# Kernel optimization log

Measured on AMD Instinct MI355X. Metric: run time of the kernel, lower is better.

## Reference

```python
import jax, jax.numpy as jnp
import numpy as np
from jax import lax

B, T, I, H = 256, 1024, 64, 128  # batch(padded_length), seq_len, input_size, hidden_size


def setup_inputs() -> dict:
    key = jax.random.key(0)
    k0, k1, k2, k3, k4 = jax.random.split(key, 5)
    s = 1.0 / np.sqrt(H)  # pytorch LSTM default init scale
    return {
        "data": jax.random.normal(k0, (B, T, I), dtype=jnp.float32),
        "W_ih": jax.random.uniform(k1, (4 * H, I), dtype=jnp.float32, minval=-s, maxval=s),
        "W_hh": jax.random.uniform(k2, (4 * H, H), dtype=jnp.float32, minval=-s, maxval=s),
        "b_ih": jax.random.uniform(k3, (4 * H,), dtype=jnp.float32, minval=-s, maxval=s),
        "b_hh": jax.random.uniform(k4, (4 * H,), dtype=jnp.float32, minval=-s, maxval=s),
    }


def reference(data, W_ih, W_hh, b_ih, b_hh):
    # data: [B, T, I]. Original permutes to [T, B, I] and runs a per-timestep
    # single-layer LSTM loop with zero initial state, collecting h_t each step.
    b, t, _ = data.shape
    h_dim = W_hh.shape[1]
    # Precompute input projection for all timesteps: [T, B, 4H]
    xs = jnp.einsum('bti,gi->tbg', data, W_ih) + b_ih + b_hh

    def step(carry, x_t):
        h, c = carry
        gates = x_t + h @ W_hh.T  # [B, 4H]
        i, f, g, o = jnp.split(gates, 4, axis=-1)  # pytorch gate order: i,f,g,o
        i = jax.nn.sigmoid(i)
        f = jax.nn.sigmoid(f)
        g = jnp.tanh(g)
        o = jax.nn.sigmoid(o)
        c = f * c + i * g
        h = o * jnp.tanh(c)
        return (h, c), h

    h0 = jnp.zeros((b, h_dim), dtype=data.dtype)
    _, hs = lax.scan(step, (h0, h0), xs)  # hs: [T, B, H]
    return jnp.transpose(hs, (1, 0, 2))  # [B, T, H]
```

## Files before the change

### kernel.cpp

```cpp
#include <hip/hip_runtime.h>


typedef _Float16 half8  __attribute__((ext_vector_type(8)));
typedef _Float16 half2t __attribute__((ext_vector_type(2)));
typedef float  floatx4  __attribute__((ext_vector_type(4)));

constexpr int Tt = 1024;
constexpr int Ii = 64;
constexpr int Hh = 128;
constexpr int CH = 16;
constexpr int NCH = Tt / CH;

__device__ __forceinline__ float fast_rcp(float x) { return __builtin_amdgcn_rcpf(x); }
__device__ __forceinline__ half2t pk16(float a, float b) {
    return __builtin_bit_cast(half2t, __builtin_amdgcn_cvt_pkrtz(a, b));
}
#define MFMA16(A, B, C) __builtin_amdgcn_mfma_f32_16x16x32_f16((A), (B), (C), 0, 0, 0)
union H8U { half8 v; half2t p[4]; };

__global__ __launch_bounds__(512, 2) void lstm_mfma4(
    const float* __restrict__ data,
    const float* __restrict__ W_ih,
    const float* __restrict__ W_hh,
    const float* __restrict__ b_ih,
    const float* __restrict__ b_hh,
    float* __restrict__ out)
{
    const int b   = blockIdx.x;
    const int t   = threadIdx.x;
    const int w   = t >> 6;
    const int l   = t & 63;
    const int col = l & 15;
    const int kg  = l >> 4;

    half8 bfh[4][4];
    half8 bfx[4][2];
    floatx4 bv[4];
#pragma unroll
    for (int g = 0; g < 4; ++g) {
        const int row = 128 * g + 16 * w + col;
        const float bias = b_ih[row] + b_hh[row];
        bv[g][0] = bias; bv[g][1] = bias; bv[g][2] = bias; bv[g][3] = bias;
        const float* wh = W_hh + (size_t)row * Hh;
        const float* wi = W_ih + (size_t)row * Ii;
#pragma unroll
        for (int s = 0; s < 4; ++s) {
            const float* src = wh + 32 * s + 8 * kg;
            const float4 f0 = ((const float4*)src)[0];
            const float4 f1 = ((const float4*)src)[1];
            H8U u;
            u.p[0] = pk16(f0.x, f0.y); u.p[1] = pk16(f0.z, f0.w);
            u.p[2] = pk16(f1.x, f1.y); u.p[3] = pk16(f1.z, f1.w);
            bfh[g][s] = u.v;
        }
#pragma unroll
        for (int s = 0; s < 2; ++s) {
            const float* src = wi + 32 * s + 8 * kg;
            const float4 f0 = ((const float4*)src)[0];
            const float4 f1 = ((const float4*)src)[1];
            H8U u;
            u.p[0] = pk16(f0.x, f0.y); u.p[1] = pk16(f0.z, f0.w);
            u.p[2] = pk16(f1.x, f1.y); u.p[3] = pk16(f1.z, f1.w);
            bfx[g][s] = u.v;
        }
    }

    __shared__ __align__(8) _Float16 hb[2][Hh];

    const float* xp  = data + (size_t)b * Tt * Ii;
    float*       opr = out  + (size_t)b * Tt * Hh + 16 * w + col;

    if (t < Hh) hb[0][t] = (_Float16)0.0f;

    const float* xbase = xp + (size_t)(l & 15) * Ii + 8 * kg;
    float4 xf0 = *(const float4*)(xbase);
    float4 xf1 = *(const float4*)(xbase + 4);
    float4 xf2 = *(const float4*)(xbase + 32);
    float4 xf3 = *(const float4*)(xbase + 36);

    float c = 0.0f;
    __syncthreads();

#pragma unroll 1
    for (int n = 0; n < NCH; ++n) {
        H8U ax0, ax1;
        ax0.p[0] = pk16(xf0.x, xf0.y); ax0.p[1] = pk16(xf0.z, xf0.w);
        ax0.p[2] = pk16(xf1.x, xf1.y); ax0.p[3] = pk16(xf1.z, xf1.w);
        ax1.p[0] = pk16(xf2.x, xf2.y); ax1.p[1] = pk16(xf2.z, xf2.w);
        ax1.p[2] = pk16(xf3.x, xf3.y); ax1.p[3] = pk16(xf3.z, xf3.w);
        floatx4 xw0 = MFMA16(ax0.v, bfx[0][0], bv[0]);
        floatx4 xw1 = MFMA16(ax0.v, bfx[1][0], bv[1]);
        floatx4 xw2 = MFMA16(ax0.v, bfx[2][0], bv[2]);
        floatx4 xw3 = MFMA16(ax0.v, bfx[3][0], bv[3]);
        xw0 = MFMA16(ax1.v, bfx[0][1], xw0);
        xw1 = MFMA16(ax1.v, bfx[1][1], xw1);
        xw2 = MFMA16(ax1.v, bfx[2][1], xw2);
        xw3 = MFMA16(ax1.v, bfx[3][1], xw3);

        {
            const int nn = (n + 1 < NCH) ? (n + 1) : n;
            const float* xb2 = xbase + (size_t)nn * CH * Ii;
            xf0 = *(const float4*)(xb2);
            xf1 = *(const float4*)(xb2 + 4);
            xf2 = *(const float4*)(xb2 + 32);
            xf3 = *(const float4*)(xb2 + 36);
        }

#define STEP(P, R, CUR)                                                       \
        {                                                                     \
            const _Float16* hbase = &hb[CUR][8 * kg];                         \
            const half8 ah0 = *(const half8*)(hbase);                         \
            const half8 ah1 = *(const half8*)(hbase + 32);                    \
            const half8 ah2 = *(const half8*)(hbase + 64);                    \
            const half8 ah3 = *(const half8*)(hbase + 96);                    \
            __builtin_amdgcn_s_setprio(1);                                    \
            floatx4 q0 = MFMA16(ah0, bfh[0][0], xw0);                  \
            floatx4 q2 = MFMA16(ah0, bfh[2][0], xw2);                  \
            q0 = MFMA16(ah1, bfh[0][1], q0);                                  \
            q2 = MFMA16(ah1, bfh[2][1], q2);                                  \
            q0 = MFMA16(ah2, bfh[0][2], q0);                                  \
            q2 = MFMA16(ah2, bfh[2][2], q2);                                  \
            q0 = MFMA16(ah3, bfh[0][3], q0);                                  \
            q2 = MFMA16(ah3, bfh[2][3], q2);                                  \
            floatx4 q1 = MFMA16(ah0, bfh[1][0], xw1);                  \
            floatx4 q3 = MFMA16(ah0, bfh[3][0], xw3);                  \
            const float gi = q0[R], gG = q2[R];                               \
            const float ig = fast_rcp(1.0f + __expf(-gi));                    \
            const float eg = __expf(-2.0f * gG);                              \
            q1 = MFMA16(ah1, bfh[1][1], q1);                                  \
            q3 = MFMA16(ah1, bfh[3][1], q3);                                  \
            const float gv = (1.0f - eg) * fast_rcp(1.0f + eg);               \
            const float igv = ig * gv;                                        \
            q1 = MFMA16(ah2, bfh[1][2], q1);                                  \
            q3 = MFMA16(ah2, bfh[3][2], q3);                                  \
            q1 = MFMA16(ah3, bfh[1][3], q1);                                  \
            q3 = MFMA16(ah3, bfh[3][3], q3);                                  \
            __builtin_amdgcn_s_setprio(0);                                    \
            const float gf = q1[R], go = q3[R];                               \
            const float fg = fast_rcp(1.0f + __expf(-gf));                    \
            const float og = fast_rcp(1.0f + __expf(-go));                    \
            c = fmaf(fg, c, igv);                                             \
            const float ec = __expf(-2.0f * c);                               \
            const float h  = og * ((1.0f - ec) * fast_rcp(1.0f + ec));        \
            if (kg == (P)) {                                                  \
                hb[(CUR) ^ 1][16 * w + col] = (_Float16)h;                    \
                *opr = h;                                                     \
            }                                                                 \
            opr += Hh;                                                        \
            asm volatile("s_waitcnt lgkmcnt(0)\n\ts_barrier" ::: "memory");   \
        }

#define PHASE(P)                                                              \
        c = __shfl(c, (l + 48) & 63);                                         \
        STEP(P, 0, 0) STEP(P, 1, 1) STEP(P, 2, 0) STEP(P, 3, 1)

        PHASE(0) PHASE(1) PHASE(2) PHASE(3)
#undef PHASE
#undef STEP
    }
}

extern "C" void kernel_launch(void* const* d_in, const int* in_sizes, int n_in,
                              void* d_out, int out_size, void* d_ws, size_t ws_size,
                              hipStream_t stream) {
    const float* data = (const float*)d_in[0];
    const float* W_ih = (const float*)d_in[1];
    const float* W_hh = (const float*)d_in[2];
    const float* b_ih = (const float*)d_in[3];
    const float* b_hh = (const float*)d_in[4];
    float* out = (float*)d_out;

    hipLaunchKernelGGL(lstm_mfma4, dim3(256), dim3(512), 0, stream,
                       data, W_ih, W_hh, b_ih, b_hh, out);
}
```

Before: 427.6 us.

## Prescale gate weights for exp2, reorder gates, software-pipeline input projection

```diff
diff --git a/kernel.cpp b/kernel.cpp
--- a/kernel.cpp
+++ b/kernel.cpp
@@ -12,13 +12,22 @@
 constexpr int NCH = Tt / CH;
 
 __device__ __forceinline__ float fast_rcp(float x) { return __builtin_amdgcn_rcpf(x); }
+__device__ __forceinline__ float exp2_(float x)    { return __builtin_amdgcn_exp2f(x); }
 __device__ __forceinline__ half2t pk16(float a, float b) {
     return __builtin_bit_cast(half2t, __builtin_amdgcn_cvt_pkrtz(a, b));
 }
 #define MFMA16(A, B, C) __builtin_amdgcn_mfma_f32_16x16x32_f16((A), (B), (C), 0, 0, 0)
 union H8U { half8 v; half2t p[4]; };
 
-__global__ __launch_bounds__(512, 2) void lstm_mfma4(
+__device__ __forceinline__ half8 cvt8(float4 a, float4 b) {
+    H8U u;
+    u.p[0] = pk16(a.x, a.y); u.p[1] = pk16(a.z, a.w);
+    u.p[2] = pk16(b.x, b.y); u.p[3] = pk16(b.z, b.w);
+    return u.v;
+}
+__device__ __forceinline__ floatx4 splat4(float a) { floatx4 r = {a, a, a, a}; return r; }
+
+__global__ __launch_bounds__(512, 1) void lstm_mfma5(
     const float* __restrict__ data,
     const float* __restrict__ W_ih,
     const float* __restrict__ W_hh,
@@ -35,12 +44,12 @@
 
     half8 bfh[4][4];
     half8 bfx[4][2];
-    floatx4 bv[4];
+    float bs[4];
 #pragma unroll
     for (int g = 0; g < 4; ++g) {
+        const float sc = (g == 2) ? -2.8853900817779268f : -1.4426950408889634f;
         const int row = 128 * g + 16 * w + col;
-        const float bias = b_ih[row] + b_hh[row];
-        bv[g][0] = bias; bv[g][1] = bias; bv[g][2] = bias; bv[g][3] = bias;
+        bs[g] = sc * (b_ih[row] + b_hh[row]);
         const float* wh = W_hh + (size_t)row * Hh;
         const float* wi = W_ih + (size_t)row * Ii;
 #pragma unroll
@@ -49,8 +58,8 @@
             const float4 f0 = ((const float4*)src)[0];
             const float4 f1 = ((const float4*)src)[1];
             H8U u;
-            u.p[0] = pk16(f0.x, f0.y); u.p[1] = pk16(f0.z, f0.w);
-            u.p[2] = pk16(f1.x, f1.y); u.p[3] = pk16(f1.z, f1.w);
+            u.p[0] = pk16(sc * f0.x, sc * f0.y); u.p[1] = pk16(sc * f0.z, sc * f0.w);
+            u.p[2] = pk16(sc * f1.x, sc * f1.y); u.p[3] = pk16(sc * f1.z, sc * f1.w);
             bfh[g][s] = u.v;
         }
 #pragma unroll
@@ -59,13 +68,13 @@
             const float4 f0 = ((const float4*)src)[0];
             const float4 f1 = ((const float4*)src)[1];
             H8U u;
-            u.p[0] = pk16(f0.x, f0.y); u.p[1] = pk16(f0.z, f0.w);
-            u.p[2] = pk16(f1.x, f1.y); u.p[3] = pk16(f1.z, f1.w);
+            u.p[0] = pk16(sc * f0.x, sc * f0.y); u.p[1] = pk16(sc * f0.z, sc * f0.w);
+            u.p[2] = pk16(sc * f1.x, sc * f1.y); u.p[3] = pk16(sc * f1.z, sc * f1.w);
             bfx[g][s] = u.v;
         }
     }
 
-    __shared__ __align__(8) _Float16 hb[2][Hh];
+    __shared__ __align__(16) _Float16 hb[2][Hh];
 
     const float* xp  = data + (size_t)b * Tt * Ii;
     float*       opr = out  + (size_t)b * Tt * Hh + 16 * w + col;
@@ -78,70 +87,67 @@
     float4 xf2 = *(const float4*)(xbase + 32);
     float4 xf3 = *(const float4*)(xbase + 36);
 
+    half8 ax0 = cvt8(xf0, xf1);
+    half8 ax1 = cvt8(xf2, xf3);
+    xf0 = *(const float4*)(xbase + CH * Ii);
+    xf1 = *(const float4*)(xbase + CH * Ii + 4);
+    xf2 = *(const float4*)(xbase + CH * Ii + 32);
+    xf3 = *(const float4*)(xbase + CH * Ii + 36);
+    floatx4 xw0 = MFMA16(ax0, bfx[0][0], splat4(bs[0]));
+    floatx4 xw1 = MFMA16(ax0, bfx[1][0], splat4(bs[1]));
+    floatx4 xw2 = MFMA16(ax0, bfx[2][0], splat4(bs[2]));
+    floatx4 xw3 = MFMA16(ax0, bfx[3][0], splat4(bs[3]));
+    xw0 = MFMA16(ax1, bfx[0][1], xw0);
+    xw1 = MFMA16(ax1, bfx[1][1], xw1);
+    xw2 = MFMA16(ax1, bfx[2][1], xw2);
+    xw3 = MFMA16(ax1, bfx[3][1], xw3);
+
+    half8 nax0, nax1;
+    floatx4 nxw0, nxw1, nxw2, nxw3;
+
     float c = 0.0f;
     __syncthreads();
 
 #pragma unroll 1
     for (int n = 0; n < NCH; ++n) {
-        H8U ax0, ax1;
-        ax0.p[0] = pk16(xf0.x, xf0.y); ax0.p[1] = pk16(xf0.z, xf0.w);
-        ax0.p[2] = pk16(xf1.x, xf1.y); ax0.p[3] = pk16(xf1.z, xf1.w);
-        ax1.p[0] = pk16(xf2.x, xf2.y); ax1.p[1] = pk16(xf2.z, xf2.w);
-        ax1.p[2] = pk16(xf3.x, xf3.y); ax1.p[3] = pk16(xf3.z, xf3.w);
-        floatx4 xw0 = MFMA16(ax0.v, bfx[0][0], bv[0]);
-        floatx4 xw1 = MFMA16(ax0.v, bfx[1][0], bv[1]);
-        floatx4 xw2 = MFMA16(ax0.v, bfx[2][0], bv[2]);
-        floatx4 xw3 = MFMA16(ax0.v, bfx[3][0], bv[3]);
-        xw0 = MFMA16(ax1.v, bfx[0][1], xw0);
-        xw1 = MFMA16(ax1.v, bfx[1][1], xw1);
-        xw2 = MFMA16(ax1.v, bfx[2][1], xw2);
-        xw3 = MFMA16(ax1.v, bfx[3][1], xw3);
-
-        {
-            const int nn = (n + 1 < NCH) ? (n + 1) : n;
-            const float* xb2 = xbase + (size_t)nn * CH * Ii;
-            xf0 = *(const float4*)(xb2);
-            xf1 = *(const float4*)(xb2 + 4);
-            xf2 = *(const float4*)(xb2 + 32);
-            xf3 = *(const float4*)(xb2 + 36);
-        }
-
-#define STEP(P, R, CUR)                                                       \
+        const float* xb2 = xbase + (size_t)((n + 2 < NCH) ? n + 2 : NCH - 1) * CH * Ii;
+
+#define STEP(P, R, CUR, XTRA)                                                 \
         {                                                                     \
             const _Float16* hbase = &hb[CUR][8 * kg];                         \
             const half8 ah0 = *(const half8*)(hbase);                         \
             const half8 ah1 = *(const half8*)(hbase + 32);                    \
             const half8 ah2 = *(const half8*)(hbase + 64);                    \
             const half8 ah3 = *(const half8*)(hbase + 96);                    \
+            XTRA;                                                             \
             __builtin_amdgcn_s_setprio(1);                                    \
-            floatx4 q0 = MFMA16(ah0, bfh[0][0], xw0);                  \
-            floatx4 q2 = MFMA16(ah0, bfh[2][0], xw2);                  \
-            q0 = MFMA16(ah1, bfh[0][1], q0);                                  \
-            q2 = MFMA16(ah1, bfh[2][1], q2);                                  \
-            q0 = MFMA16(ah2, bfh[0][2], q0);                                  \
-            q2 = MFMA16(ah2, bfh[2][2], q2);                                  \
-            q0 = MFMA16(ah3, bfh[0][3], q0);                                  \
-            q2 = MFMA16(ah3, bfh[2][3], q2);                                  \
-            floatx4 q1 = MFMA16(ah0, bfh[1][0], xw1);                  \
-            floatx4 q3 = MFMA16(ah0, bfh[3][0], xw3);                  \
-            const float gi = q0[R], gG = q2[R];                               \
-            const float ig = fast_rcp(1.0f + __expf(-gi));                    \
-            const float eg = __expf(-2.0f * gG);                              \
-            q1 = MFMA16(ah1, bfh[1][1], q1);                                  \
-            q3 = MFMA16(ah1, bfh[3][1], q3);                                  \
+            floatx4 qf = MFMA16(ah0, bfh[1][0], xw1);                  \
+            floatx4 qg = MFMA16(ah0, bfh[2][0], xw2);                  \
+            qf = MFMA16(ah1, bfh[1][1], qf);                                  \
+            qg = MFMA16(ah1, bfh[2][1], qg);                                  \
+            qf = MFMA16(ah2, bfh[1][2], qf);                                  \
+            qg = MFMA16(ah2, bfh[2][2], qg);                                  \
+            qf = MFMA16(ah3, bfh[1][3], qf);                                  \
+            qg = MFMA16(ah3, bfh[2][3], qg);                                  \
+            floatx4 qi = MFMA16(ah0, bfh[0][0], xw0);                  \
+            floatx4 qo = MFMA16(ah0, bfh[3][0], xw3);                  \
+            const float fg = fast_rcp(1.0f + exp2_(qf[R]));                   \
+            const float eg = exp2_(qg[R]);                                    \
+            qi = MFMA16(ah1, bfh[0][1], qi);                                  \
+            qo = MFMA16(ah1, bfh[3][1], qo);                                  \
+            const float fc = fg * c;                                          \
             const float gv = (1.0f - eg) * fast_rcp(1.0f + eg);               \
-            const float igv = ig * gv;                                        \
-            q1 = MFMA16(ah2, bfh[1][2], q1);                                  \
-            q3 = MFMA16(ah2, bfh[3][2], q3);                                  \
-            q1 = MFMA16(ah3, bfh[1][3], q1);                                  \
-            q3 = MFMA16(ah3, bfh[3][3], q3);                                  \
+            qi = MFMA16(ah2, bfh[0][2], qi);                                  \
+            qo = MFMA16(ah2, bfh[3][2], qo);                                  \
+            qi = MFMA16(ah3, bfh[0][3], qi);                                  \
+            qo = MFMA16(ah3, bfh[3][3], qo);                                  \
             __builtin_amdgcn_s_setprio(0);                                    \
-            const float gf = q1[R], go = q3[R];                               \
-            const float fg = fast_rcp(1.0f + __expf(-gf));                    \
-            const float og = fast_rcp(1.0f + __expf(-go));                    \
-            c = fmaf(fg, c, igv);                                             \
-            const float ec = __expf(-2.0f * c);                               \
-            const float h  = og * ((1.0f - ec) * fast_rcp(1.0f + ec));        \
+            const float ig = fast_rcp(1.0f + exp2_(qi[R]));                   \
+            c = fmaf(ig, gv, fc);                                             \
+            const float ec = exp2_(-2.8853900817779268f * c);                 \
+            const float tc = (1.0f - ec) * fast_rcp(1.0f + ec);               \
+            const float og = fast_rcp(1.0f + exp2_(qo[R]));                   \
+            const float h  = og * tc;                                         \
             if (kg == (P)) {                                                  \
                 hb[(CUR) ^ 1][16 * w + col] = (_Float16)h;                    \
                 *opr = h;                                                     \
@@ -150,13 +156,34 @@
             asm volatile("s_waitcnt lgkmcnt(0)\n\ts_barrier" ::: "memory");   \
         }
 
-#define PHASE(P)                                                              \
+#define PHASE(P, X0, X1, X2, X3)                                              \
         c = __shfl(c, (l + 48) & 63);                                         \
-        STEP(P, 0, 0) STEP(P, 1, 1) STEP(P, 2, 0) STEP(P, 3, 1)
-
-        PHASE(0) PHASE(1) PHASE(2) PHASE(3)
+        STEP(P, 0, 0, X0) STEP(P, 1, 1, X1) STEP(P, 2, 0, X2) STEP(P, 3, 1, X3)
+
+        PHASE(0,
+              nax0 = cvt8(xf0, xf1),
+              nax1 = cvt8(xf2, xf3),
+              nxw0 = MFMA16(nax0, bfx[0][0], splat4(bs[0])),
+              nxw1 = MFMA16(nax0, bfx[1][0], splat4(bs[1])))
+        PHASE(1,
+              nxw2 = MFMA16(nax0, bfx[2][0], splat4(bs[2])),
+              nxw3 = MFMA16(nax0, bfx[3][0], splat4(bs[3])),
+              nxw0 = MFMA16(nax1, bfx[0][1], nxw0),
+              nxw1 = MFMA16(nax1, bfx[1][1], nxw1))
+        PHASE(2,
+              nxw2 = MFMA16(nax1, bfx[2][1], nxw2),
+              nxw3 = MFMA16(nax1, bfx[3][1], nxw3),
+              xf0 = *(const float4*)(xb2),
+              xf1 = *(const float4*)(xb2 + 4))
+        PHASE(3,
+              xf2 = *(const float4*)(xb2 + 32),
+              xf3 = *(const float4*)(xb2 + 36),
+              (void)0,
+              (void)0)
 #undef PHASE
 #undef STEP
+
+        xw0 = nxw0; xw1 = nxw1; xw2 = nxw2; xw3 = nxw3;
     }
 }
 
@@ -170,6 +197,6 @@
     const float* b_hh = (const float*)d_in[4];
     float* out = (float*)d_out;
 
-    hipLaunchKernelGGL(lstm_mfma4, dim3(256), dim3(512), 0, stream,
+    hipLaunchKernelGGL(lstm_mfma5, dim3(256), dim3(512), 0, stream,
                        data, W_ih, W_hh, b_ih, b_hh, out);
 }
```

Result: faster. 416.9 us (-2.5%).
